# Kernel optimization log

Measured on AMD Instinct MI355X. Metric: run time of the kernel, lower is better.

Reference implementation:

```python
import jax, jax.numpy as jnp
import numpy as np
import math

N_CLASSES = 91
BBOX_W = (10.0, 10.0, 5.0, 5.0)
NMS_T = 0.5
SCORE_T = 0.05
DET_K = 100          # detections_per_img
MIN_SIZE = 0.01
CLAMP = math.log(1000.0 / 16.0)
NEG = -1e9


def decode(deltas, boxes):
    # torchvision BoxCoder.decode with weights BBOX_W, xyxy boxes
    wx, wy, ww, wh = BBOX_W
    w = boxes[..., 2] - boxes[..., 0]
    h = boxes[..., 3] - boxes[..., 1]
    cx = boxes[..., 0] + 0.5 * w
    cy = boxes[..., 1] + 0.5 * h
    dx = deltas[..., 0] / wx
    dy = deltas[..., 1] / wy
    dw = jnp.minimum(deltas[..., 2] / ww, CLAMP)
    dh = jnp.minimum(deltas[..., 3] / wh, CLAMP)
    pcx = dx * w + cx
    pcy = dy * h + cy
    pw = jnp.exp(dw) * w
    ph = jnp.exp(dh) * h
    return jnp.stack([pcx - 0.5 * pw, pcy - 0.5 * ph,
                      pcx + 0.5 * pw, pcy + 0.5 * ph], -1)


def iou_1many(b, boxes):
    x1 = jnp.maximum(b[0], boxes[:, 0]); y1 = jnp.maximum(b[1], boxes[:, 1])
    x2 = jnp.minimum(b[2], boxes[:, 2]); y2 = jnp.minimum(b[3], boxes[:, 3])
    inter = jnp.clip(x2 - x1, 0.0) * jnp.clip(y2 - y1, 0.0)
    a1 = (b[2] - b[0]) * (b[3] - b[1])
    a2 = (boxes[:, 2] - boxes[:, 0]) * (boxes[:, 3] - boxes[:, 1])
    return inter / jnp.maximum(a1 + a2 - inter, 1e-9)


def nms_img(boxes, scores, labels, valid):
    # batched_nms via per-class coordinate offsets; sequential greedy NMS,
    # fixed DET_K iterations (top-detections_per_img kept), padded with keep=False
    maxc = jnp.max(jnp.where(valid[:, None], boxes, 0.0))
    ob = boxes + (labels.astype(boxes.dtype) * (maxc + 1.0))[:, None]

    def step(act, _):
        i = jnp.argmax(act)
        keep = act[i] > NEG / 2
        iou = iou_1many(ob[i], ob)
        act = jnp.where(keep & (iou > NMS_T), NEG, act)
        act = act.at[i].set(NEG)
        return act, (i, keep)

    init = jnp.where(valid, scores, NEG)
    _, (idx, keep) = jax.lax.scan(step, init, None, length=DET_K)
    return idx, keep


def _forward(hw, class_logits, pred_bbox_deltas, proposals):
    H, W = hw
    N, P, C = class_logits.shape
    probs = jax.nn.softmax(class_logits, -1)
    fg = probs[..., 1:]                                  # drop background col
    scores = jnp.max(fg, -1)
    labels = jnp.argmax(fg, -1) + 1                      # [N,P] in 1..C-1
    deltas = pred_bbox_deltas.reshape(N, P, C, 4)
    sel = jnp.take_along_axis(deltas, labels[..., None, None], axis=2)[:, :, 0, :]
    boxes = decode(sel, proposals)
    boxes = jnp.stack([jnp.clip(boxes[..., 0], 0.0, W),
                       jnp.clip(boxes[..., 1], 0.0, H),
                       jnp.clip(boxes[..., 2], 0.0, W),
                       jnp.clip(boxes[..., 3], 0.0, H)], -1)
    ws = boxes[..., 2] - boxes[..., 0]
    hs = boxes[..., 3] - boxes[..., 1]
    valid = (ws >= MIN_SIZE) & (hs >= MIN_SIZE) & (scores > SCORE_T)
    idx, keep = jax.vmap(nms_img)(boxes, scores, labels, valid)
    bg = jnp.take_along_axis(boxes, idx[..., None], 1)   # [N,K,4]
    sg = jnp.take_along_axis(scores, idx, 1)
    lg = jnp.take_along_axis(labels, idx, 1)
    scores_out = jnp.where(keep, sg, 0.0)
    labels_out = jnp.where(keep, lg, 0)
    boxes_out = jnp.where(keep[..., None], bg, 0.0)
    return labels_out, scores_out, boxes_out


def setup_inputs() -> dict:
    key = jax.random.key(0)
    k1, k2, k3, k4 = jax.random.split(key, 4)
    N, P, C, H, W = 8, 4000, N_CLASSES, 800, 800
    class_logits = jax.random.normal(k1, (N, P, C), jnp.float32) * 2.0
    pred_bbox_deltas = jax.random.normal(k2, (N, P, C * 4), jnp.float32) * 0.5
    ctr = jax.random.uniform(k3, (N, P, 2), minval=0.0, maxval=800.0)
    wh = jax.random.uniform(k4, (N, P, 2), minval=16.0, maxval=300.0)
    proposals = jnp.concatenate([jnp.clip(ctr - 0.5 * wh, 0.0, 800.0),
                                 jnp.clip(ctr + 0.5 * wh, 0.0, 800.0)], -1)
    images = jnp.zeros((N, 3, H, W), jnp.float32)
    return {"images": images, "class_logits": class_logits,
            "pred_bbox_deltas": pred_bbox_deltas, "proposals": proposals}


def reference(images, class_logits, pred_bbox_deltas, proposals):
    return _forward(images.shape[-2:], class_logits, pred_bbox_deltas, proposals)
```

## Files before the change

kernel.cpp:

```cpp
#include <hip/hip_runtime.h>
#include <hip/hip_fp16.h>
#include <math.h>

#define NIMG 8
#define PNUM 4000
#define CNUM 91
#define NLAB (CNUM - 1)
#define DETK 100
#define LCAP 128
#define TOTALQ (NIMG * PNUM)
#define NEGV  -1000000000.0
#define NEGH  -500000000.0
#define CLAMP64 4.1351665567423558

#define WS3_ACT   0
#define WS3_BH4   256000
#define WS3_LAB   768000
#define WS3_CNT   832000
#define WS3_LKEY  836096
#define WS3_LJ    1573376
#define WS3_LBOX  1942016
#define WS3_NEED  4891136

#if defined(__has_builtin)
# if __has_builtin(__builtin_amdgcn_readlane)
#  define RDLANE(v,l) __builtin_amdgcn_readlane((int)(v),(l))
# endif
#endif
#ifndef RDLANE
# define RDLANE(v,l) __shfl((int)(v),(l))
#endif

__device__ __forceinline__ unsigned long long rdlane64(unsigned long long v, int l) {
    const unsigned int lo = (unsigned int)RDLANE((unsigned int)v, l);
    const unsigned int hi = (unsigned int)RDLANE((unsigned int)(v >> 32), l);
    return ((unsigned long long)hi << 32) | lo;
}

extern "C" __global__ __launch_bounds__(256)
void k_softmax(const float* __restrict__ logits,
               double* __restrict__ w_act,
               unsigned short* __restrict__ w_lab,
               unsigned int* __restrict__ w_cnt)
{
    if (blockIdx.x == 0) {
        #pragma unroll
        for (int t = 0; t < 4; ++t)
            w_cnt[threadIdx.x * 4 + t] = 0u;
    }

    const int lane  = threadIdx.x & 63;
    const int wavid = threadIdx.x >> 6;
    const int g     = lane >> 3;
    const int hl    = lane & 7;
    const int wid   = blockIdx.x * 32 + wavid * 8 + g;

    const float* lg = logits + (long)wid * CNUM;

    float lv[12];
    #pragma unroll
    for (int k = 0; k < 11; ++k) lv[k] = lg[hl + 8 * k];
    const bool hasLast = hl < 3;
    lv[11] = hasLast ? lg[88 + hl] : 0.0f;

    float mx = lv[0];
    #pragma unroll
    for (int k = 1; k < 11; ++k) mx = fmaxf(mx, lv[k]);
    if (hasLast) mx = fmaxf(mx, lv[11]);

    float bv = -INFINITY; int bc = 0x7fffffff;
    #pragma unroll
    for (int k = 0; k < 11; ++k) {
        const int c = hl + 8 * k;
        if (c >= 1 && lv[k] > bv) { bv = lv[k]; bc = c; }
    }
    if (hasLast && lv[11] > bv) { bv = lv[11]; bc = 88 + hl; }

    #pragma unroll
    for (int s = 4; s; s >>= 1) {
        mx = fmaxf(mx, __shfl_xor(mx, s));
        const float ov = __shfl_xor(bv, s);
        const int   oc = __shfl_xor(bc, s);
        if (ov > bv || (ov == bv && oc < bc)) { bv = ov; bc = oc; }
    }

    double sum = 0.0;
    #pragma unroll
    for (int k = 0; k < 11; ++k) sum += exp((double)lv[k] - (double)mx);
    if (hasLast) sum += exp((double)lv[11] - (double)mx);
    #pragma unroll
    for (int s = 4; s; s >>= 1) sum += __shfl_xor(sum, s);

    if (hl == 0) {
        w_act[wid] = exp((double)bv - (double)mx) / sum;
        w_lab[wid] = (unsigned short)bc;
    }
}

extern "C" __global__ __launch_bounds__(256)
void k_decode(const float* __restrict__ deltas,
              const float* __restrict__ props,
              double* __restrict__ w_act,
              float4* __restrict__ w_bh4,
              const unsigned short* __restrict__ w_lab,
              unsigned int* __restrict__ w_cnt,
              unsigned long long* __restrict__ w_lkey,
              int* __restrict__ w_lj,
              double* __restrict__ w_lbox)
{
    const int wid = blockIdx.x * 256 + threadIdx.x;
    if (wid >= TOTALQ) return;

    const double score = w_act[wid];
    const int    label = (int)w_lab[wid];

    const float4 pr = *reinterpret_cast<const float4*>(props + (long)wid * 4);
    const double x1p = (double)pr.x, y1p = (double)pr.y;
    const double x2p = (double)pr.z, y2p = (double)pr.w;
    const double w  = x2p - x1p, h = y2p - y1p;
    const double cx = x1p + 0.5 * w, cy = y1p + 0.5 * h;

    const float4 dl = *reinterpret_cast<const float4*>(
        deltas + (long)wid * (CNUM * 4) + label * 4);
    const double dx = (double)dl.x / 10.0;
    const double dy = (double)dl.y / 10.0;
    const double dw = fmin((double)dl.z / 5.0, CLAMP64);
    const double dh = fmin((double)dl.w / 5.0, CLAMP64);

    const double pcx = dx * w + cx;
    const double pcy = dy * h + cy;
    const double pw  = exp(dw) * w;
    const double ph  = exp(dh) * h;

    double x1 = pcx - 0.5 * pw, y1 = pcy - 0.5 * ph;
    double x2 = pcx + 0.5 * pw, y2 = pcy + 0.5 * ph;
    x1 = fmin(fmax(x1, 0.0), 800.0);
    y1 = fmin(fmax(y1, 0.0), 800.0);
    x2 = fmin(fmax(x2, 0.0), 800.0);
    y2 = fmin(fmax(y2, 0.0), 800.0);

    const bool valid = ((x2 - x1) >= 0.01) && ((y2 - y1) >= 0.01) && (score > 0.05);

    if (valid) {
        w_bh4[wid] = make_float4((float)x1, (float)y1, (float)x2, (float)y2);
        const int img = wid / PNUM;
        const int j   = wid - img * PNUM;
        const unsigned int slot = atomicAdd(&w_cnt[img * CNUM + label], 1u);
        if (slot < LCAP) {
            const long ls = (long)(img * NLAB + label - 1) * LCAP + slot;
            w_lkey[ls] = (unsigned long long)__double_as_longlong(score);
            w_lj[ls]   = j;
            double* bx = w_lbox + ls * 4;
            bx[0] = x1; bx[1] = y1; bx[2] = x2; bx[3] = y2;
        }
    } else {
        w_act[wid] = NEGV;
    }
}

extern "C" __global__ __launch_bounds__(64)
void k_nms6(double* w_act,
            const unsigned int* __restrict__ w_cnt,
            const unsigned long long* __restrict__ w_lkey,
            const int* __restrict__ w_lj,
            const double* __restrict__ w_lbox)
{
    __shared__ unsigned long long skey[LCAP];
    __shared__ int    sj[LCAP];
    __shared__ double sx1[LCAP], sy1[LCAP], sx2[LCAP], sy2[LCAP];
    __shared__ unsigned short perm[LCAP];
    __shared__ double tx1[LCAP], ty1[LCAP], tx2[LCAP], ty2[LCAP];
    __shared__ int    tj[LCAP];

    const int img   = blockIdx.x / NLAB;
    const int label = 1 + (blockIdx.x % NLAB);
    const int lane  = threadIdx.x;
    const long base = (long)img * PNUM;

    const int m = min((int)w_cnt[img * CNUM + label], LCAP);
    if (m <= 1) return;

    const long lb = (long)(img * NLAB + label - 1) * LCAP;
    const int  s2 = lane + 64;
    const bool h1v = lane < m;
    const bool h2v = s2 < m;

    unsigned long long k1 = 0, k2 = 0; int j1 = 0, j2 = 0;
    double2 ba1 = {0,0}, bb1 = {0,0}, ba2 = {0,0}, bb2 = {0,0};
    if (h1v) {
        k1 = w_lkey[lb + lane]; j1 = w_lj[lb + lane];
        ba1 = *reinterpret_cast<const double2*>(w_lbox + (lb + lane) * 4);
        bb1 = *reinterpret_cast<const double2*>(w_lbox + (lb + lane) * 4 + 2);
    }
    if (h2v) {
        k2 = w_lkey[lb + s2]; j2 = w_lj[lb + s2];
        ba2 = *reinterpret_cast<const double2*>(w_lbox + (lb + s2) * 4);
        bb2 = *reinterpret_cast<const double2*>(w_lbox + (lb + s2) * 4 + 2);
    }
    if (h1v) { skey[lane] = k1; sj[lane] = j1;
               sx1[lane] = ba1.x; sy1[lane] = ba1.y; sx2[lane] = bb1.x; sy2[lane] = bb1.y; }
    if (h2v) { skey[s2] = k2; sj[s2] = j2;
               sx1[s2] = ba2.x; sy1[s2] = ba2.y; sx2[s2] = bb2.x; sy2[s2] = bb2.y; }
    __syncthreads();

    int r1 = 0, r2 = 0;
    for (int q = 0; q < m; ++q) {
        const unsigned long long kq = skey[q];
        const int jq = sj[q];
        r1 += (int)(h1v && ((kq > k1) || (kq == k1 && jq < j1)));
        r2 += (int)(h2v && ((kq > k2) || (kq == k2 && jq < j2)));
    }
    if (h1v) perm[r1] = (unsigned short)lane;
    if (h2v) perm[r2] = (unsigned short)s2;
    __syncthreads();

    if (h1v) { const int sp = perm[lane];
        tx1[lane] = sx1[sp]; ty1[lane] = sy1[sp];
        tx2[lane] = sx2[sp]; ty2[lane] = sy2[sp]; tj[lane] = sj[sp]; }
    if (h2v) { const int sp = perm[s2];
        tx1[s2] = sx1[sp]; ty1[s2] = sy1[sp];
        tx2[s2] = sx2[sp]; ty2[s2] = sy2[sp]; tj[s2] = sj[sp]; }
    __syncthreads();

    double p1x1=0, p1y1=0, p1x2=0, p1y2=0, ar1=0;
    double p2x1=0, p2y1=0, p2x2=0, p2y2=0, ar2=0;
    if (h1v) { p1x1=tx1[lane]; p1y1=ty1[lane]; p1x2=tx2[lane]; p1y2=ty2[lane];
               ar1 = (p1x2-p1x1)*(p1y2-p1y1); }
    if (h2v) { p2x1=tx1[s2]; p2y1=ty1[s2]; p2x2=tx2[s2]; p2y2=ty2[s2];
               ar2 = (p2x2-p2x1)*(p2y2-p2y1); }
    unsigned long long rA0=0, rA1=0, rB0=0, rB1=0;
    for (int q = 0; q < m; ++q) {
        const double qx1 = tx1[q], qy1 = ty1[q], qx2 = tx2[q], qy2 = ty2[q];
        const double a2  = (qx2 - qx1) * (qy2 - qy1);
        if (h1v && q != lane) {
            const double ix = fmin(p1x2, qx2) - fmax(p1x1, qx1);
            const double iy = fmin(p1y2, qy2) - fmax(p1y1, qy1);
            const double inter = fmax(ix, 0.0) * fmax(iy, 0.0);
            const double uni = fmax(ar1 + a2 - inter, 1e-9);
            if (inter / uni > 0.5) { if (q < 64) rA0 |= 1ull << q; else rA1 |= 1ull << (q - 64); }
        }
        if (h2v && q != s2) {
            const double ix = fmin(p2x2, qx2) - fmax(p2x1, qx1);
            const double iy = fmin(p2y2, qy2) - fmax(p2y1, qy1);
            const double inter = fmax(ix, 0.0) * fmax(iy, 0.0);
            const double uni = fmax(ar2 + a2 - inter, 1e-9);
            if (inter / uni > 0.5) { if (q < 64) rB0 |= 1ull << q; else rB1 |= 1ull << (q - 64); }
        }
    }

    unsigned long long sa = 0, sb = 0;
    for (int i = 0; i < m; ++i) {
        unsigned long long w0, w1;
        bool kept;
        if (i < 64) {
            w0 = rdlane64(rA0, i); w1 = rdlane64(rA1, i);
            kept = !((sa >> i) & 1ull);
        } else {
            w0 = rdlane64(rB0, i - 64); w1 = rdlane64(rB1, i - 64);
            kept = !((sb >> (i - 64)) & 1ull);
        }
        if (kept) { sa |= w0; sb |= w1; }
    }

    if (h1v && ((sa >> lane) & 1ull)) w_act[base + tj[lane]] = NEGV;
    if (h2v && ((sb >> lane) & 1ull)) w_act[base + tj[s2]]   = NEGV;
}

#define NBINS 2304
#define CHW   36
#define NCHK  64

extern "C" __global__ __launch_bounds__(1024)
void k_topk(const double* __restrict__ w_act,
            const float4* __restrict__ w_bh4,
            const unsigned short* __restrict__ w_lab,
            float* __restrict__ out)
{
    __shared__ int hist[NBINS];
    __shared__ int sT, scnt;
    __shared__ unsigned long long cKey[1024];
    __shared__ int cIdx[1024];
    __shared__ unsigned long long rKey[DETK];
    __shared__ int rIdx[DETK];

    const int n = blockIdx.x;
    const int tid = threadIdx.x;
    const long base = (long)n * PNUM;
    const unsigned long long KBASE = 0x3FA999999999999Aull >> 43;

    for (int i = tid; i < NBINS; i += 1024) hist[i] = 0;
    if (tid < DETK) rIdx[tid] = -1;
    if (tid == 0) { sT = 0; scnt = 0; }
    __syncthreads();

    for (int j = tid; j < PNUM; j += 1024) {
        const double a = w_act[base + j];
        if (a > 0.0) {
            const unsigned long long k = (unsigned long long)__double_as_longlong(a);
            int b = (int)((k >> 43) - KBASE);
            b = min(max(b, 0), NBINS - 1);
            atomicAdd(&hist[b], 1);
        }
    }
    __syncthreads();

    if (tid < NCHK) {
        int s = 0;
        for (int b = 0; b < CHW; ++b) s += hist[tid * CHW + b];
        int suf = s;
        #pragma unroll
        for (int off = 1; off < NCHK; off <<= 1) {
            const int o = __shfl_down(suf, off);
            suf += (tid + off < NCHK) ? o : 0;
        }
        const unsigned long long mk = __ballot(suf >= DETK);
        if (mk != 0ull) {
            const int ch  = 63 - __clzll(mk);
            const int Shi = (ch < NCHK - 1) ? __shfl(suf, ch + 1) : 0;
            int W = 0;
            if (tid < CHW) for (int b = tid; b < CHW; ++b) W += hist[ch * CHW + b];
            const unsigned long long mk2 = __ballot((tid < CHW) && (W + Shi >= DETK));
            if (tid == 0) sT = ch * CHW + (63 - __clzll(mk2));
        }
    }
    __syncthreads();
    const int T = sT;

    for (int j = tid; j < PNUM; j += 1024) {
        const double a = w_act[base + j];
        if (a > 0.0) {
            const unsigned long long k = (unsigned long long)__double_as_longlong(a);
            int b = (int)((k >> 43) - KBASE);
            b = min(max(b, 0), NBINS - 1);
            if (b >= T) {
                const int p = atomicAdd(&scnt, 1);
                if (p < 1024) { cKey[p] = k; cIdx[p] = j; }
            }
        }
    }
    __syncthreads();
    const int cnt = min(scnt, 1024);

    for (int s = tid; s < cnt; s += 1024) {
        const unsigned long long ks = cKey[s];
        const int is = cIdx[s];
        int rank = 0;
        for (int q = 0; q < cnt; ++q) {
            const unsigned long long kq = cKey[q];
            rank += (int)((kq > ks) || (kq == ks && cIdx[q] < is));
        }
        if (rank < DETK) { rKey[rank] = ks; rIdx[rank] = is; }
    }
    __syncthreads();

    if (tid < DETK) {
        const int o = n * DETK + tid;
        const int idx = rIdx[tid];
        const bool kp = (idx >= 0);
        float lab = 0.f, sc = 0.f, b0 = 0.f, b1 = 0.f, b2 = 0.f, b3 = 0.f;
        if (kp) {
            lab = (float)w_lab[base + idx];
            sc  = (float)__longlong_as_double((long long)rKey[tid]);
            const float4 bh = w_bh4[base + idx];
            b0 = bh.x; b1 = bh.y; b2 = bh.z; b3 = bh.w;
        }
        out[o]               = lab;
        out[NIMG * DETK + o] = sc;
        out[2 * NIMG * DETK + o * 4 + 0] = b0;
        out[2 * NIMG * DETK + o * 4 + 1] = b1;
        out[2 * NIMG * DETK + o * 4 + 2] = b2;
        out[2 * NIMG * DETK + o * 4 + 3] = b3;
    }
}

extern "C" __global__ __launch_bounds__(1024)
void k_fused(const float* __restrict__ logits,
             const float* __restrict__ deltas,
             const float* __restrict__ props,
             float* __restrict__ out)
{
    __shared__ float   bh0[PNUM], bh1[PNUM], bh2[PNUM], bh3[PNUM];
    __shared__ __half  bl0[PNUM], bl1[PNUM], bl2[PNUM], bl3[PNUM];
    __shared__ double  act[PNUM];
    __shared__ unsigned short slab[PNUM];
    __shared__ double  redV[16];
    __shared__ int     redI[16];
    __shared__ double  pbox[4];
    __shared__ int     pidx, pkeep, plab;
    __shared__ int     kidx[DETK], kkeep[DETK];
    __shared__ double  kscore[DETK];
    __shared__ double  kbox[DETK][4];

    const int n   = blockIdx.x;
    const int tid = threadIdx.x;

    for (int j = tid; j < PNUM; j += 1024) {
        const long q = (long)n * PNUM + j;
        const float* lg = logits + q * CNUM;
        float ml = lg[0];
        float bv = lg[1];
        int   lab = 1;
        for (int c = 1; c < CNUM; ++c) {
            const float v = lg[c];
            ml = fmaxf(ml, v);
            if (c >= 2 && v > bv) { bv = v; lab = c; }
        }
        const double m = (double)ml;
        double sum = 0.0;
        for (int c = 0; c < CNUM; ++c) sum += exp((double)lg[c] - m);
        const double score = exp((double)bv - m) / sum;

        const float* pr = props + q * 4;
        const double x1p = (double)pr[0], y1p = (double)pr[1];
        const double x2p = (double)pr[2], y2p = (double)pr[3];
        const double w  = x2p - x1p, h = y2p - y1p;
        const double cx = x1p + 0.5 * w, cy = y1p + 0.5 * h;
        const float* dl = deltas + q * (CNUM * 4) + lab * 4;
        const double dx = (double)dl[0] / 10.0;
        const double dy = (double)dl[1] / 10.0;
        const double dw = fmin((double)dl[2] / 5.0, CLAMP64);
        const double dh = fmin((double)dl[3] / 5.0, CLAMP64);
        const double pcx = dx * w + cx;
        const double pcy = dy * h + cy;
        const double pw  = exp(dw) * w;
        const double ph  = exp(dh) * h;
        double x1 = pcx - 0.5 * pw, y1 = pcy - 0.5 * ph;
        double x2 = pcx + 0.5 * pw, y2 = pcy + 0.5 * ph;
        x1 = fmin(fmax(x1, 0.0), 800.0);
        y1 = fmin(fmax(y1, 0.0), 800.0);
        x2 = fmin(fmax(x2, 0.0), 800.0);
        y2 = fmin(fmax(y2, 0.0), 800.0);
        const bool valid = ((x2 - x1) >= 0.01) && ((y2 - y1) >= 0.01) && (score > 0.05);
        act[j]  = valid ? score : NEGV;
        slab[j] = (unsigned short)lab;
        const float h0 = (float)x1, h1 = (float)y1, h2 = (float)x2, h3 = (float)y2;
        bh0[j] = h0; bh1[j] = h1; bh2[j] = h2; bh3[j] = h3;
        bl0[j] = __float2half((float)(x1 - (double)h0));
        bl1[j] = __float2half((float)(y1 - (double)h1));
        bl2[j] = __float2half((float)(x2 - (double)h2));
        bl3[j] = __float2half((float)(y2 - (double)h3));
    }
    __syncthreads();

    for (int k = 0; k < DETK; ++k) {
        double bv = -INFINITY;
        int    bi = 0x7fffffff;
        #pragma unroll
        for (int t = 0; t < 4; ++t) {
            const int j = tid + t * 1024;
            if (j < PNUM) {
                const double v = act[j];
                if (v > bv) { bv = v; bi = j; }
            }
        }
        #pragma unroll
        for (int s = 32; s; s >>= 1) {
            const double ov = __shfl_xor(bv, s);
            const int    oi = __shfl_xor(bi, s);
            if (ov > bv || (ov == bv && oi < bi)) { bv = ov; bi = oi; }
        }
        if ((tid & 63) == 0) { redV[tid >> 6] = bv; redI[tid >> 6] = bi; }
        __syncthreads();
        if (tid < 64) {
            bv = (tid < 16) ? redV[tid] : -INFINITY;
            bi = (tid < 16) ? redI[tid] : 0x7fffffff;
            #pragma unroll
            for (int s = 8; s; s >>= 1) {
                const double ov = __shfl_xor(bv, s);
                const int    oi = __shfl_xor(bi, s);
                if (ov > bv || (ov == bv && oi < bi)) { bv = ov; bi = oi; }
            }
            if (tid == 0) {
                const int kp = (bv > NEGH) ? 1 : 0;
                pidx = bi; pkeep = kp; plab = (int)slab[bi];
                kidx[k] = bi; kkeep[k] = kp; kscore[k] = bv;
                const double b0 = (double)bh0[bi] + (double)__half2float(bl0[bi]);
                const double b1 = (double)bh1[bi] + (double)__half2float(bl1[bi]);
                const double b2 = (double)bh2[bi] + (double)__half2float(bl2[bi]);
                const double b3 = (double)bh3[bi] + (double)__half2float(bl3[bi]);
                pbox[0] = b0; pbox[1] = b1; pbox[2] = b2; pbox[3] = b3;
                kbox[k][0] = b0; kbox[k][1] = b1; kbox[k][2] = b2; kbox[k][3] = b3;
            }
        }
        __syncthreads();

        const int    pick = pidx;
        const int    kp   = pkeep;
        const int    pl   = plab;
        const double px1 = pbox[0], py1 = pbox[1], px2 = pbox[2], py2 = pbox[3];
        const double a1  = (px2 - px1) * (py2 - py1);
        #pragma unroll
        for (int t = 0; t < 4; ++t) {
            const int j = tid + t * 1024;
            if (j >= PNUM) break;
            if (j == pick) { act[j] = NEGV; continue; }
            if (!kp) continue;
            if ((int)slab[j] != pl) continue;
            if (act[j] <= NEGH) continue;
            const double qx1 = (double)bh0[j] + (double)__half2float(bl0[j]);
            const double qy1 = (double)bh1[j] + (double)__half2float(bl1[j]);
            const double qx2 = (double)bh2[j] + (double)__half2float(bl2[j]);
            const double qy2 = (double)bh3[j] + (double)__half2float(bl3[j]);
            const double ix = fmin(px2, qx2) - fmax(px1, qx1);
            const double iy = fmin(py2, qy2) - fmax(py1, qy1);
            const double inter = fmax(ix, 0.0) * fmax(iy, 0.0);
            const double a2  = (qx2 - qx1) * (qy2 - qy1);
            const double uni = fmax(a1 + a2 - inter, 1e-9);
            if (inter / uni > 0.5) act[j] = NEGV;
        }
        __syncthreads();
    }

    if (tid < DETK) {
        const int kp = kkeep[tid];
        const int o  = n * DETK + tid;
        out[o]               = kp ? (float)slab[kidx[tid]] : 0.0f;
        out[NIMG * DETK + o] = kp ? (float)kscore[tid] : 0.0f;
        #pragma unroll
        for (int i = 0; i < 4; ++i)
            out[2 * NIMG * DETK + o * 4 + i] = kp ? (float)kbox[tid][i] : 0.0f;
    }
}

extern "C" void kernel_launch(void* const* d_in, const int* in_sizes, int n_in,
                              void* d_out, int out_size, void* d_ws, size_t ws_size,
                              hipStream_t stream)
{
    const float* logits = (const float*)d_in[1];
    const float* deltas = (const float*)d_in[2];
    const float* props  = (const float*)d_in[3];
    float* out = (float*)d_out;
    char* ws = (char*)d_ws;

    if (ws_size >= (size_t)WS3_NEED) {
        double*             w_act  = (double*)(ws + WS3_ACT);
        float4*             w_bh4  = (float4*)(ws + WS3_BH4);
        unsigned short*     w_lab  = (unsigned short*)(ws + WS3_LAB);
        unsigned int*       w_cnt  = (unsigned int*)(ws + WS3_CNT);
        unsigned long long* w_lkey = (unsigned long long*)(ws + WS3_LKEY);
        int*                w_lj   = (int*)(ws + WS3_LJ);
        double*             w_lbox = (double*)(ws + WS3_LBOX);

        hipLaunchKernelGGL(k_softmax, dim3(TOTALQ / 32), dim3(256), 0, stream,
                           logits, w_act, w_lab, w_cnt);
        hipLaunchKernelGGL(k_decode, dim3((TOTALQ + 255) / 256), dim3(256), 0, stream,
                           deltas, props, w_act, w_bh4, w_lab,
                           w_cnt, w_lkey, w_lj, w_lbox);
        hipLaunchKernelGGL(k_nms6, dim3(NIMG * NLAB), dim3(64), 0, stream,
                           w_act, w_cnt, w_lkey, w_lj, w_lbox);
        hipLaunchKernelGGL(k_topk, dim3(NIMG), dim3(1024), 0, stream,
                           w_act, w_bh4, w_lab, out);
    } else {
        hipLaunchKernelGGL(k_fused, dim3(NIMG), dim3(1024), 0, stream,
                           logits, deltas, props, out);
    }
}
```

Measured before the change: 64.83 us.

## Fuse softmax with decode and per-class NMS with top-k to cut launches

Merges the softmax and box-decode kernels into one kernel that stages scores and labels in shared memory. Replaces the global atomic per-class bucketing and the separate NMS kernel with in-block bucketing (histogram, prefix sum, scatter) inside the top-k kernel. Each of 16 wavefronts then runs NMS on one class at a time, using shared memory and register lane-reads. This drops two kernel launches and the global atomics and bucket buffers. The cost is that NMS now runs on only 8 blocks instead of 720, which serializes the per-class work and may extend the tail.

```diff
diff --git a/kernel.cpp b/kernel.cpp
--- a/kernel.cpp
+++ b/kernel.cpp
@@ -5,7 +5,6 @@
 #define NIMG 8
 #define PNUM 4000
 #define CNUM 91
-#define NLAB (CNUM - 1)
 #define DETK 100
 #define LCAP 128
 #define TOTALQ (NIMG * PNUM)
@@ -13,14 +12,11 @@
 #define NEGH  -500000000.0
 #define CLAMP64 4.1351665567423558
 
-#define WS3_ACT   0
-#define WS3_BH4   256000
-#define WS3_LAB   768000
-#define WS3_CNT   832000
-#define WS3_LKEY  836096
-#define WS3_LJ    1573376
-#define WS3_LBOX  1942016
-#define WS3_NEED  4891136
+#define W_ACT 0
+#define W_BH4 256000
+#define W_LAB 768000
+#define W_B64 832000
+#define WS_NEED 1856000
 
 #if defined(__has_builtin)
 # if __has_builtin(__builtin_amdgcn_readlane)
@@ -37,91 +33,81 @@
     return ((unsigned long long)hi << 32) | lo;
 }
 
-extern "C" __global__ __launch_bounds__(256)
-void k_softmax(const float* __restrict__ logits,
-               double* __restrict__ w_act,
-               unsigned short* __restrict__ w_lab,
-               unsigned int* __restrict__ w_cnt)
+extern "C" __global__ __launch_bounds__(128)
+void k_sm_decode(const float* __restrict__ logits,
+                 const float* __restrict__ deltas,
+                 const float* __restrict__ props,
+                 double* __restrict__ w_act,
+                 float4* __restrict__ w_bh4,
+                 unsigned short* __restrict__ w_lab,
+                 double* __restrict__ w_b64)
 {
-    if (blockIdx.x == 0) {
-        #pragma unroll
-        for (int t = 0; t < 4; ++t)
-            w_cnt[threadIdx.x * 4 + t] = 0u;
-    }
-
-    const int lane  = threadIdx.x & 63;
-    const int wavid = threadIdx.x >> 6;
-    const int g     = lane >> 3;
-    const int hl    = lane & 7;
-    const int wid   = blockIdx.x * 32 + wavid * 8 + g;
-
-    const float* lg = logits + (long)wid * CNUM;
-
-    float lv[12];
-    #pragma unroll
-    for (int k = 0; k < 11; ++k) lv[k] = lg[hl + 8 * k];
-    const bool hasLast = hl < 3;
-    lv[11] = hasLast ? lg[88 + hl] : 0.0f;
-
-    float mx = lv[0];
-    #pragma unroll
-    for (int k = 1; k < 11; ++k) mx = fmaxf(mx, lv[k]);
-    if (hasLast) mx = fmaxf(mx, lv[11]);
-
-    float bv = -INFINITY; int bc = 0x7fffffff;
-    #pragma unroll
-    for (int k = 0; k < 11; ++k) {
-        const int c = hl + 8 * k;
-        if (c >= 1 && lv[k] > bv) { bv = lv[k]; bc = c; }
-    }
-    if (hasLast && lv[11] > bv) { bv = lv[11]; bc = 88 + hl; }
-
-    #pragma unroll
-    for (int s = 4; s; s >>= 1) {
-        mx = fmaxf(mx, __shfl_xor(mx, s));
-        const float ov = __shfl_xor(bv, s);
-        const int   oc = __shfl_xor(bc, s);
-        if (ov > bv || (ov == bv && oc < bc)) { bv = ov; bc = oc; }
-    }
-
-    double sum = 0.0;
-    #pragma unroll
-    for (int k = 0; k < 11; ++k) sum += exp((double)lv[k] - (double)mx);
-    if (hasLast) sum += exp((double)lv[11] - (double)mx);
-    #pragma unroll
-    for (int s = 4; s; s >>= 1) sum += __shfl_xor(sum, s);
-
-    if (hl == 0) {
-        w_act[wid] = exp((double)bv - (double)mx) / sum;
-        w_lab[wid] = (unsigned short)bc;
-    }
-}
-
-extern "C" __global__ __launch_bounds__(256)
-void k_decode(const float* __restrict__ deltas,
-              const float* __restrict__ props,
-              double* __restrict__ w_act,
-              float4* __restrict__ w_bh4,
-              const unsigned short* __restrict__ w_lab,
-              unsigned int* __restrict__ w_cnt,
-              unsigned long long* __restrict__ w_lkey,
-              int* __restrict__ w_lj,
-              double* __restrict__ w_lbox)
-{
-    const int wid = blockIdx.x * 256 + threadIdx.x;
-    if (wid >= TOTALQ) return;
-
-    const double score = w_act[wid];
-    const int    label = (int)w_lab[wid];
-
-    const float4 pr = *reinterpret_cast<const float4*>(props + (long)wid * 4);
+    __shared__ double sS[128];
+    __shared__ unsigned short sL[128];
+
+    const int tid  = threadIdx.x;
+    const int wv   = tid >> 6, lane = tid & 63;
+    const int g    = lane >> 3, hl = lane & 7;
+    const int blockbase = blockIdx.x * 128;
+
+    for (int pass = 0; pass < 8; ++pass) {
+        const int  local = wv * 64 + pass * 8 + g;
+        const long wid   = blockbase + local;
+        const float* lg  = logits + wid * CNUM;
+
+        float lv[12];
+        #pragma unroll
+        for (int k = 0; k < 11; ++k) lv[k] = lg[hl + 8 * k];
+        const bool hasLast = hl < 3;
+        lv[11] = hasLast ? lg[88 + hl] : 0.0f;
+
+        float mx = lv[0];
+        #pragma unroll
+        for (int k = 1; k < 11; ++k) mx = fmaxf(mx, lv[k]);
+        if (hasLast) mx = fmaxf(mx, lv[11]);
+
+        float bv = -INFINITY; int bc = 0x7fffffff;
+        #pragma unroll
+        for (int k = 0; k < 11; ++k) {
+            const int c = hl + 8 * k;
+            if (c >= 1 && lv[k] > bv) { bv = lv[k]; bc = c; }
+        }
+        if (hasLast && lv[11] > bv) { bv = lv[11]; bc = 88 + hl; }
+
+        #pragma unroll
+        for (int s = 4; s; s >>= 1) {
+            mx = fmaxf(mx, __shfl_xor(mx, s));
+            const float ov = __shfl_xor(bv, s);
+            const int   oc = __shfl_xor(bc, s);
+            if (ov > bv || (ov == bv && oc < bc)) { bv = ov; bc = oc; }
+        }
+
+        double sum = 0.0;
+        #pragma unroll
+        for (int k = 0; k < 11; ++k) sum += exp((double)lv[k] - (double)mx);
+        if (hasLast) sum += exp((double)lv[11] - (double)mx);
+        #pragma unroll
+        for (int s = 4; s; s >>= 1) sum += __shfl_xor(sum, s);
+
+        if (hl == 0) {
+            sS[local] = exp((double)bv - (double)mx) / sum;
+            sL[local] = (unsigned short)bc;
+        }
+    }
+    __syncthreads();
+
+    const long wid   = blockbase + tid;
+    const double score = sS[tid];
+    const int    label = (int)sL[tid];
+
+    const float4 pr = *reinterpret_cast<const float4*>(props + wid * 4);
     const double x1p = (double)pr.x, y1p = (double)pr.y;
     const double x2p = (double)pr.z, y2p = (double)pr.w;
     const double w  = x2p - x1p, h = y2p - y1p;
     const double cx = x1p + 0.5 * w, cy = y1p + 0.5 * h;
 
     const float4 dl = *reinterpret_cast<const float4*>(
-        deltas + (long)wid * (CNUM * 4) + label * 4);
+        deltas + wid * (CNUM * 4) + label * 4);
     const double dx = (double)dl.x / 10.0;
     const double dy = (double)dl.y / 10.0;
     const double dw = fmin((double)dl.z / 5.0, CLAMP64);
@@ -141,129 +127,13 @@
 
     const bool valid = ((x2 - x1) >= 0.01) && ((y2 - y1) >= 0.01) && (score > 0.05);
 
+    w_act[wid] = valid ? score : NEGV;
+    w_lab[wid] = (unsigned short)label;
     if (valid) {
         w_bh4[wid] = make_float4((float)x1, (float)y1, (float)x2, (float)y2);
-        const int img = wid / PNUM;
-        const int j   = wid - img * PNUM;
-        const unsigned int slot = atomicAdd(&w_cnt[img * CNUM + label], 1u);
-        if (slot < LCAP) {
-            const long ls = (long)(img * NLAB + label - 1) * LCAP + slot;
-            w_lkey[ls] = (unsigned long long)__double_as_longlong(score);
-            w_lj[ls]   = j;
-            double* bx = w_lbox + ls * 4;
-            bx[0] = x1; bx[1] = y1; bx[2] = x2; bx[3] = y2;
-        }
-    } else {
-        w_act[wid] = NEGV;
-    }
-}
-
-extern "C" __global__ __launch_bounds__(64)
-void k_nms6(double* w_act,
-            const unsigned int* __restrict__ w_cnt,
-            const unsigned long long* __restrict__ w_lkey,
-            const int* __restrict__ w_lj,
-            const double* __restrict__ w_lbox)
-{
-    __shared__ unsigned long long skey[LCAP];
-    __shared__ int    sj[LCAP];
-    __shared__ double sx1[LCAP], sy1[LCAP], sx2[LCAP], sy2[LCAP];
-    __shared__ unsigned short perm[LCAP];
-    __shared__ double tx1[LCAP], ty1[LCAP], tx2[LCAP], ty2[LCAP];
-    __shared__ int    tj[LCAP];
-
-    const int img   = blockIdx.x / NLAB;
-    const int label = 1 + (blockIdx.x % NLAB);
-    const int lane  = threadIdx.x;
-    const long base = (long)img * PNUM;
-
-    const int m = min((int)w_cnt[img * CNUM + label], LCAP);
-    if (m <= 1) return;
-
-    const long lb = (long)(img * NLAB + label - 1) * LCAP;
-    const int  s2 = lane + 64;
-    const bool h1v = lane < m;
-    const bool h2v = s2 < m;
-
-    unsigned long long k1 = 0, k2 = 0; int j1 = 0, j2 = 0;
-    double2 ba1 = {0,0}, bb1 = {0,0}, ba2 = {0,0}, bb2 = {0,0};
-    if (h1v) {
-        k1 = w_lkey[lb + lane]; j1 = w_lj[lb + lane];
-        ba1 = *reinterpret_cast<const double2*>(w_lbox + (lb + lane) * 4);
-        bb1 = *reinterpret_cast<const double2*>(w_lbox + (lb + lane) * 4 + 2);
-    }
-    if (h2v) {
-        k2 = w_lkey[lb + s2]; j2 = w_lj[lb + s2];
-        ba2 = *reinterpret_cast<const double2*>(w_lbox + (lb + s2) * 4);
-        bb2 = *reinterpret_cast<const double2*>(w_lbox + (lb + s2) * 4 + 2);
-    }
-    if (h1v) { skey[lane] = k1; sj[lane] = j1;
-               sx1[lane] = ba1.x; sy1[lane] = ba1.y; sx2[lane] = bb1.x; sy2[lane] = bb1.y; }
-    if (h2v) { skey[s2] = k2; sj[s2] = j2;
-               sx1[s2] = ba2.x; sy1[s2] = ba2.y; sx2[s2] = bb2.x; sy2[s2] = bb2.y; }
-    __syncthreads();
-
-    int r1 = 0, r2 = 0;
-    for (int q = 0; q < m; ++q) {
-        const unsigned long long kq = skey[q];
-        const int jq = sj[q];
-        r1 += (int)(h1v && ((kq > k1) || (kq == k1 && jq < j1)));
-        r2 += (int)(h2v && ((kq > k2) || (kq == k2 && jq < j2)));
-    }
-    if (h1v) perm[r1] = (unsigned short)lane;
-    if (h2v) perm[r2] = (unsigned short)s2;
-    __syncthreads();
-
-    if (h1v) { const int sp = perm[lane];
-        tx1[lane] = sx1[sp]; ty1[lane] = sy1[sp];
-        tx2[lane] = sx2[sp]; ty2[lane] = sy2[sp]; tj[lane] = sj[sp]; }
-    if (h2v) { const int sp = perm[s2];
-        tx1[s2] = sx1[sp]; ty1[s2] = sy1[sp];
-        tx2[s2] = sx2[sp]; ty2[s2] = sy2[sp]; tj[s2] = sj[sp]; }
-    __syncthreads();
-
-    double p1x1=0, p1y1=0, p1x2=0, p1y2=0, ar1=0;
-    double p2x1=0, p2y1=0, p2x2=0, p2y2=0, ar2=0;
-    if (h1v) { p1x1=tx1[lane]; p1y1=ty1[lane]; p1x2=tx2[lane]; p1y2=ty2[lane];
-               ar1 = (p1x2-p1x1)*(p1y2-p1y1); }
-    if (h2v) { p2x1=tx1[s2]; p2y1=ty1[s2]; p2x2=tx2[s2]; p2y2=ty2[s2];
-               ar2 = (p2x2-p2x1)*(p2y2-p2y1); }
-    unsigned long long rA0=0, rA1=0, rB0=0, rB1=0;
-    for (int q = 0; q < m; ++q) {
-        const double qx1 = tx1[q], qy1 = ty1[q], qx2 = tx2[q], qy2 = ty2[q];
-        const double a2  = (qx2 - qx1) * (qy2 - qy1);
-        if (h1v && q != lane) {
-            const double ix = fmin(p1x2, qx2) - fmax(p1x1, qx1);
-            const double iy = fmin(p1y2, qy2) - fmax(p1y1, qy1);
-            const double inter = fmax(ix, 0.0) * fmax(iy, 0.0);
-            const double uni = fmax(ar1 + a2 - inter, 1e-9);
-            if (inter / uni > 0.5) { if (q < 64) rA0 |= 1ull << q; else rA1 |= 1ull << (q - 64); }
-        }
-        if (h2v && q != s2) {
-            const double ix = fmin(p2x2, qx2) - fmax(p2x1, qx1);
-            const double iy = fmin(p2y2, qy2) - fmax(p2y1, qy1);
-            const double inter = fmax(ix, 0.0) * fmax(iy, 0.0);
-            const double uni = fmax(ar2 + a2 - inter, 1e-9);
-            if (inter / uni > 0.5) { if (q < 64) rB0 |= 1ull << q; else rB1 |= 1ull << (q - 64); }
-        }
-    }
-
-    unsigned long long sa = 0, sb = 0;
-    for (int i = 0; i < m; ++i) {
-        unsigned long long w0, w1;
-        bool kept;
-        if (i < 64) {
-            w0 = rdlane64(rA0, i); w1 = rdlane64(rA1, i);
-            kept = !((sa >> i) & 1ull);
-        } else {
-            w0 = rdlane64(rB0, i - 64); w1 = rdlane64(rB1, i - 64);
-            kept = !((sb >> (i - 64)) & 1ull);
-        }
-        if (kept) { sa |= w0; sb |= w1; }
-    }
-
-    if (h1v && ((sa >> lane) & 1ull)) w_act[base + tj[lane]] = NEGV;
-    if (h2v && ((sb >> lane) & 1ull)) w_act[base + tj[s2]]   = NEGV;
+        double* bx = w_b64 + wid * 4;
+        bx[0] = x1; bx[1] = y1; bx[2] = x2; bx[3] = y2;
+    }
 }
 
 #define NBINS 2304
@@ -271,30 +141,163 @@
 #define NCHK  64
 
 extern "C" __global__ __launch_bounds__(1024)
-void k_topk(const double* __restrict__ w_act,
-            const float4* __restrict__ w_bh4,
-            const unsigned short* __restrict__ w_lab,
-            float* __restrict__ out)
+void k_nms_topk(const double* __restrict__ w_act,
+                const float4* __restrict__ w_bh4,
+                const unsigned short* __restrict__ w_lab,
+                const double* __restrict__ w_b64,
+                float* __restrict__ out)
 {
+    __shared__ double actL[PNUM];
+    __shared__ unsigned short labL[PNUM];
+    __shared__ unsigned short list[PNUM];
+    __shared__ int cnt[96], off[96], cur[96];
+    __shared__ double wx1[16][LCAP], wy1[16][LCAP],
+                      wx2[16][LCAP], wy2[16][LCAP];
+    __shared__ unsigned short wjj[16][LCAP];
     __shared__ int hist[NBINS];
-    __shared__ int sT, scnt;
     __shared__ unsigned long long cKey[1024];
     __shared__ int cIdx[1024];
     __shared__ unsigned long long rKey[DETK];
     __shared__ int rIdx[DETK];
-
-    const int n = blockIdx.x;
+    __shared__ int sT, scnt;
+
+    const int n   = blockIdx.x;
     const int tid = threadIdx.x;
     const long base = (long)n * PNUM;
     const unsigned long long KBASE = 0x3FA999999999999Aull >> 43;
 
+    for (int j = tid; j < PNUM; j += 1024) {
+        actL[j] = w_act[base + j];
+        labL[j] = w_lab[base + j];
+    }
+    if (tid < 96) { cnt[tid] = 0; cur[tid] = 0; }
     for (int i = tid; i < NBINS; i += 1024) hist[i] = 0;
     if (tid < DETK) rIdx[tid] = -1;
     if (tid == 0) { sT = 0; scnt = 0; }
     __syncthreads();
 
+    for (int j = tid; j < PNUM; j += 1024)
+        if (actL[j] > 0.0) atomicAdd(&cnt[labL[j]], 1);
+    __syncthreads();
+
+    if (tid < 64) {
+        const int l1 = tid + 1;
+        const int v = cnt[l1];
+        int p = v;
+        #pragma unroll
+        for (int d = 1; d < 64; d <<= 1) {
+            const int o = __shfl_up(p, d);
+            if (tid >= d) p += o;
+        }
+        off[l1] = p - v;
+        const int tot1 = __shfl(p, 63);
+        const int l2 = 65 + tid;
+        const int v2 = (l2 < CNUM) ? cnt[l2] : 0;
+        int p2 = v2;
+        #pragma unroll
+        for (int d = 1; d < 64; d <<= 1) {
+            const int o = __shfl_up(p2, d);
+            if (tid >= d) p2 += o;
+        }
+        if (l2 < CNUM) off[l2] = tot1 + p2 - v2;
+    }
+    __syncthreads();
+
+    for (int j = tid; j < PNUM; j += 1024)
+        if (actL[j] > 0.0) {
+            const int l = labL[j];
+            const int p = atomicAdd(&cur[l], 1);
+            list[off[l] + p] = (unsigned short)j;
+        }
+    __syncthreads();
+
+    const int w = tid >> 6, lane = tid & 63;
+    for (int l = 1 + w; l < CNUM; l += 16) {
+        const int m = min(cnt[l], LCAP);
+        if (m < 2) continue;
+        const int sbase = off[l];
+        const int s2 = lane + 64;
+        const bool h1v = lane < m, h2v = s2 < m;
+
+        int j1 = 0, j2 = 0;
+        unsigned long long k1 = 0, k2 = 0;
+        double a1x1=0,a1y1=0,a1x2=0,a1y2=0;
+        double a2x1=0,a2y1=0,a2x2=0,a2y2=0;
+        if (h1v) {
+            j1 = list[sbase + lane];
+            k1 = (unsigned long long)__double_as_longlong(actL[j1]);
+            const double* bp = w_b64 + (base + j1) * 4;
+            a1x1 = bp[0]; a1y1 = bp[1]; a1x2 = bp[2]; a1y2 = bp[3];
+        }
+        if (h2v) {
+            j2 = list[sbase + s2];
+            k2 = (unsigned long long)__double_as_longlong(actL[j2]);
+            const double* bp = w_b64 + (base + j2) * 4;
+            a2x1 = bp[0]; a2y1 = bp[1]; a2x2 = bp[2]; a2y2 = bp[3];
+        }
+
+        int r1 = 0, r2 = 0;
+        for (int q = 0; q < m; ++q) {
+            unsigned long long kq; int jq;
+            if (q < 64) { kq = rdlane64(k1, q); jq = RDLANE(j1, q); }
+            else        { kq = rdlane64(k2, q - 64); jq = RDLANE(j2, q - 64); }
+            r1 += (int)(h1v && ((kq > k1) || (kq == k1 && jq < j1)));
+            r2 += (int)(h2v && ((kq > k2) || (kq == k2 && jq < j2)));
+        }
+        if (h1v) { wx1[w][r1]=a1x1; wy1[w][r1]=a1y1; wx2[w][r1]=a1x2; wy2[w][r1]=a1y2;
+                   wjj[w][r1] = (unsigned short)j1; }
+        if (h2v) { wx1[w][r2]=a2x1; wy1[w][r2]=a2y1; wx2[w][r2]=a2x2; wy2[w][r2]=a2y2;
+                   wjj[w][r2] = (unsigned short)j2; }
+        asm volatile("s_waitcnt lgkmcnt(0)" ::: "memory");
+
+        double p1x1=0,p1y1=0,p1x2=0,p1y2=0,ar1=0;
+        double p2x1=0,p2y1=0,p2x2=0,p2y2=0,ar2=0;
+        if (h1v) { p1x1=wx1[w][lane]; p1y1=wy1[w][lane]; p1x2=wx2[w][lane]; p1y2=wy2[w][lane];
+                   ar1 = (p1x2-p1x1)*(p1y2-p1y1); }
+        if (h2v) { p2x1=wx1[w][s2]; p2y1=wy1[w][s2]; p2x2=wx2[w][s2]; p2y2=wy2[w][s2];
+                   ar2 = (p2x2-p2x1)*(p2y2-p2y1); }
+        unsigned long long rA0=0, rA1=0, rB0=0, rB1=0;
+        for (int q = 0; q < m; ++q) {
+            const double qx1 = wx1[w][q], qy1 = wy1[w][q];
+            const double qx2 = wx2[w][q], qy2 = wy2[w][q];
+            const double a2  = (qx2 - qx1) * (qy2 - qy1);
+            if (h1v && q != lane) {
+                const double ix = fmin(p1x2, qx2) - fmax(p1x1, qx1);
+                const double iy = fmin(p1y2, qy2) - fmax(p1y1, qy1);
+                const double inter = fmax(ix, 0.0) * fmax(iy, 0.0);
+                const double uni = fmax(ar1 + a2 - inter, 1e-9);
+                if (inter / uni > 0.5) { if (q < 64) rA0 |= 1ull << q; else rA1 |= 1ull << (q - 64); }
+            }
+            if (h2v && q != s2) {
+                const double ix = fmin(p2x2, qx2) - fmax(p2x1, qx1);
+                const double iy = fmin(p2y2, qy2) - fmax(p2y1, qy1);
+                const double inter = fmax(ix, 0.0) * fmax(iy, 0.0);
+                const double uni = fmax(ar2 + a2 - inter, 1e-9);
+                if (inter / uni > 0.5) { if (q < 64) rB0 |= 1ull << q; else rB1 |= 1ull << (q - 64); }
+            }
+        }
+
+        unsigned long long sa = 0, sb = 0;
+        for (int i = 0; i < m; ++i) {
+            unsigned long long w0, w1;
+            bool kept;
+            if (i < 64) {
+                w0 = rdlane64(rA0, i); w1 = rdlane64(rA1, i);
+                kept = !((sa >> i) & 1ull);
+            } else {
+                w0 = rdlane64(rB0, i - 64); w1 = rdlane64(rB1, i - 64);
+                kept = !((sb >> (i - 64)) & 1ull);
+            }
+            if (kept) { sa |= w0; sb |= w1; }
+        }
+
+        if (h1v && ((sa >> lane) & 1ull)) actL[wjj[w][lane]] = NEGV;
+        if (h2v && ((sb >> lane) & 1ull)) actL[wjj[w][s2]]   = NEGV;
+    }
+    __syncthreads();
+
     for (int j = tid; j < PNUM; j += 1024) {
-        const double a = w_act[base + j];
+        const double a = actL[j];
         if (a > 0.0) {
             const unsigned long long k = (unsigned long long)__double_as_longlong(a);
             int b = (int)((k >> 43) - KBASE);
@@ -309,9 +312,9 @@
         for (int b = 0; b < CHW; ++b) s += hist[tid * CHW + b];
         int suf = s;
         #pragma unroll
-        for (int off = 1; off < NCHK; off <<= 1) {
-            const int o = __shfl_down(suf, off);
-            suf += (tid + off < NCHK) ? o : 0;
+        for (int o2 = 1; o2 < NCHK; o2 <<= 1) {
+            const int o = __shfl_down(suf, o2);
+            suf += (tid + o2 < NCHK) ? o : 0;
         }
         const unsigned long long mk = __ballot(suf >= DETK);
         if (mk != 0ull) {
@@ -327,7 +330,7 @@
     const int T = sT;
 
     for (int j = tid; j < PNUM; j += 1024) {
-        const double a = w_act[base + j];
+        const double a = actL[j];
         if (a > 0.0) {
             const unsigned long long k = (unsigned long long)__double_as_longlong(a);
             int b = (int)((k >> 43) - KBASE);
@@ -339,13 +342,13 @@
         }
     }
     __syncthreads();
-    const int cnt = min(scnt, 1024);
-
-    for (int s = tid; s < cnt; s += 1024) {
+    const int cnt2 = min(scnt, 1024);
+
+    for (int s = tid; s < cnt2; s += 1024) {
         const unsigned long long ks = cKey[s];
         const int is = cIdx[s];
         int rank = 0;
-        for (int q = 0; q < cnt; ++q) {
+        for (int q = 0; q < cnt2; ++q) {
             const unsigned long long kq = cKey[q];
             rank += (int)((kq > ks) || (kq == ks && cIdx[q] < is));
         }
@@ -359,7 +362,7 @@
         const bool kp = (idx >= 0);
         float lab = 0.f, sc = 0.f, b0 = 0.f, b1 = 0.f, b2 = 0.f, b3 = 0.f;
         if (kp) {
-            lab = (float)w_lab[base + idx];
+            lab = (float)labL[idx];
             sc  = (float)__longlong_as_double((long long)rKey[tid]);
             const float4 bh = w_bh4[base + idx];
             b0 = bh.x; b1 = bh.y; b2 = bh.z; b3 = bh.w;
@@ -532,24 +535,16 @@
     float* out = (float*)d_out;
     char* ws = (char*)d_ws;
 
-    if (ws_size >= (size_t)WS3_NEED) {
-        double*             w_act  = (double*)(ws + WS3_ACT);
-        float4*             w_bh4  = (float4*)(ws + WS3_BH4);
-        unsigned short*     w_lab  = (unsigned short*)(ws + WS3_LAB);
-        unsigned int*       w_cnt  = (unsigned int*)(ws + WS3_CNT);
-        unsigned long long* w_lkey = (unsigned long long*)(ws + WS3_LKEY);
-        int*                w_lj   = (int*)(ws + WS3_LJ);
-        double*             w_lbox = (double*)(ws + WS3_LBOX);
-
-        hipLaunchKernelGGL(k_softmax, dim3(TOTALQ / 32), dim3(256), 0, stream,
-                           logits, w_act, w_lab, w_cnt);
-        hipLaunchKernelGGL(k_decode, dim3((TOTALQ + 255) / 256), dim3(256), 0, stream,
-                           deltas, props, w_act, w_bh4, w_lab,
-                           w_cnt, w_lkey, w_lj, w_lbox);
-        hipLaunchKernelGGL(k_nms6, dim3(NIMG * NLAB), dim3(64), 0, stream,
-                           w_act, w_cnt, w_lkey, w_lj, w_lbox);
-        hipLaunchKernelGGL(k_topk, dim3(NIMG), dim3(1024), 0, stream,
-                           w_act, w_bh4, w_lab, out);
+    if (ws_size >= (size_t)WS_NEED) {
+        double*         w_act = (double*)(ws + W_ACT);
+        float4*         w_bh4 = (float4*)(ws + W_BH4);
+        unsigned short* w_lab = (unsigned short*)(ws + W_LAB);
+        double*         w_b64 = (double*)(ws + W_B64);
+
+        hipLaunchKernelGGL(k_sm_decode, dim3(TOTALQ / 128), dim3(128), 0, stream,
+                           logits, deltas, props, w_act, w_bh4, w_lab, w_b64);
+        hipLaunchKernelGGL(k_nms_topk, dim3(NIMG), dim3(1024), 0, stream,
+                           w_act, w_bh4, w_lab, w_b64, out);
     } else {
         hipLaunchKernelGGL(k_fused, dim3(NIMG), dim3(1024), 0, stream,
                            logits, deltas, props, out);
```

Result: slower. 217.3 us (+235.2%).
